# Kernel tuning notes

Hardware: AMD Instinct MI355X
Metric: run time of the kernel (lower is better)

The kernel has to match this reference:

```python
import jax, jax.numpy as jnp
import numpy as np

TOKEN_SELF_ATTN_VALUE = -50000.0
EPS_NORM = 1e-12
EPS_SCATTER = 1e-5
COMMITMENT = 1e-4


def _l2norm(x):
    return x / jnp.maximum(jnp.linalg.norm(x, axis=-1, keepdims=True), EPS_NORM)


def _shift(x):
    # relative-position shift, faithful to the torch `shift` helper
    # x: [..., i, j] -> [..., i, j]
    *pre, i, j = x.shape
    x = jnp.concatenate([x, jnp.zeros((*pre, i, i), x.dtype)], axis=-1)  # [..., i, i+j]
    l = i + j - 1
    x = x.reshape(*pre, i * (i + j))
    pad = (-x.shape[-1]) % l
    x = jnp.concatenate([x, jnp.zeros((*pre, pad), x.dtype)], axis=-1)
    x = x.reshape(*pre, -1, l)
    return x[..., :i, i - 1:]


def setup_inputs() -> dict:
    key = jax.random.key(0)
    k1, k2, k3, k4 = jax.random.split(key, 4)
    b, h, t, d = 4, 8, 8192, 64
    c, wsz = 64, 128
    qk = jax.random.normal(k1, (b, h, t, d), jnp.float32)
    v = jax.random.normal(k2, (b, h, t, d), jnp.float32)
    means = jax.random.normal(k3, (h, c, d), jnp.float32)
    means = _l2norm(means)  # trained kmeans means are unit-normalized
    rel_w = jax.random.normal(k4, (wsz, h, d), jnp.float32) * 0.02
    return {"qk": qk, "v": v, "means": means, "rel_w": rel_w}


def reference(qk, v, means, rel_w):
    b, h, t, d = qk.shape
    c = means.shape[1]
    wsz = min(rel_w.shape[0], t)

    # ---- kmeans routing (eval path: no iterations, fixed means) ----
    k_routing = _l2norm(qk)                                   # [b,h,t,d]
    dists = jnp.einsum('bhld,hcd->bhlc', k_routing, means)    # cosine sims
    buckets = jnp.argmax(dists, axis=-1)                      # [b,h,t]
    # top-wsz tokens per cluster, sorted ascending (matches topk -> sort -> transpose)
    _, idx = jax.lax.top_k(jnp.swapaxes(dists, -1, -2), wsz)  # [b,h,c,wsz]
    indices = jnp.sort(idx, axis=-1).reshape(b, h, c * wsz)   # [b,h,c*wsz]

    # commitment loss against routed means (means is a non-trainable buffer)
    routed_means = means[jnp.arange(h)[None, :, None], buckets]  # [b,h,t,d]
    loss = jnp.mean((k_routing - routed_means) ** 2) * COMMITMENT

    # ---- gather routed windows ----
    qk_g = jnp.take_along_axis(qk, indices[..., None], axis=2).reshape(b, h, c, wsz, d)
    v_g = jnp.take_along_axis(v, indices[..., None], axis=2).reshape(b, h, c, wsz, d)
    q = qk_g
    k = _l2norm(qk_g)

    scale = d ** -0.5
    dots = jnp.einsum('bhnid,bhnjd->bhnij', q, k) * scale     # [b,h,c,wsz,wsz]
    rel = jnp.einsum('bhnid,jhd->bhnij', q, rel_w) * scale
    dots = dots + _shift(rel)

    # token cannot attend to itself within its window
    eye = jnp.eye(wsz, dtype=bool)
    dots = jnp.where(eye, TOKEN_SELF_ATTN_VALUE, dots)

    attn = jax.nn.softmax(dots, axis=-1)
    bo = jnp.einsum('bhnij,bhnjd->bhnid', attn, v_g).reshape(b, h, c * wsz, d)

    # ---- scatter-mean back to original token positions ----
    def scat(idx1, src1):  # idx1: [N], src1: [N,d]
        num = jnp.zeros((t, d), src1.dtype).at[idx1].add(src1)
        den = jnp.zeros((t, d), src1.dtype).at[idx1].add(jnp.ones_like(src1))
        return num / (den + EPS_SCATTER)

    out = jax.vmap(jax.vmap(scat))(indices, bo)               # [b,h,t,d]
    return out, loss
```

## Files before the change

### kernel.cpp

```cpp
#include <hip/hip_runtime.h>
#include <hip/hip_bf16.h>
#include <math.h>

#define NB 4
#define NH 8
#define TT 8192
#define DD 64
#define NC 64
#define WW 128
#define BHN 32
#define SCALE 0.125f
#define INVCAP 24
#define DTPB 64

typedef __bf16  bf16x8 __attribute__((ext_vector_type(8)));
typedef __bf16  bf16x4 __attribute__((ext_vector_type(4)));
typedef float   f32x4  __attribute__((ext_vector_type(4)));
typedef unsigned long long u64;
typedef unsigned int u32;

#define MFMA(a, b, c) __builtin_amdgcn_mfma_f32_16x16x32_bf16((a), (b), (c), 0, 0, 0)

__device__ __forceinline__ u32 monokey(float f) {
    const u32 u = __float_as_uint(f);
    return u ^ (((u32)((int)u >> 31)) | 0x80000000u);
}

__global__ __launch_bounds__(256) void k_prep(
    const float* __restrict__ rel_w, const float* __restrict__ means,
    __bf16* __restrict__ relb, __bf16* __restrict__ msp, float* __restrict__ mn2)
{
    const int b = blockIdx.x, tid = threadIdx.x;
    if (b < 64) {
        const int i = b * 256 + tid;
        const float4 v = ((const float4*)rel_w)[i];
        bf16x4 o;
        o[0] = (__bf16)v.x; o[1] = (__bf16)v.y; o[2] = (__bf16)v.z; o[3] = (__bf16)v.w;
        *(bf16x4*)(relb + i * 4) = o;
    } else {
        const int i = (b - 64) * 256 + tid;
        const float4 v = ((const float4*)means)[i];
        __bf16* mh = msp;
        __bf16* mm = msp + 32768;
        __bf16* ml = msp + 65536;
        float x[4] = {v.x, v.y, v.z, v.w};
        bf16x4 oh, om, ol;
        float ssq = 0.f;
#pragma unroll
        for (int j = 0; j < 4; j++) {
            ssq = fmaf(x[j], x[j], ssq);
            const __bf16 hh_ = (__bf16)x[j];
            const float r1 = x[j] - (float)hh_;
            const __bf16 mm_ = (__bf16)r1;
            const float r2 = r1 - (float)mm_;
            oh[j] = hh_; om[j] = mm_; ol[j] = (__bf16)r2;
        }
        *(bf16x4*)(mh + i * 4) = oh;
        *(bf16x4*)(mm + i * 4) = om;
        *(bf16x4*)(ml + i * 4) = ol;
#pragma unroll
        for (int o = 1; o < 16; o <<= 1) ssq += __shfl_xor(ssq, o);
        if ((tid & 15) == 0) mn2[i >> 4] = ssq;
    }
}

#define QD_ADDR(row, gi) (((row) << 6) + ((((gi) ^ ((row) & 7))) << 3))

__global__ __launch_bounds__(256) void k_dists(
    const float* __restrict__ qk, const __bf16* __restrict__ msp,
    const float* __restrict__ mn2g, u32* __restrict__ keys,
    double* __restrict__ lossa)
{
    __shared__ __attribute__((aligned(16))) __bf16 qh[64 * 64], qm[64 * 64], ql[64 * 64];
    __shared__ __attribute__((aligned(16))) __bf16 ah[64 * 64], am[64 * 64], al[64 * 64];
    __shared__ float invS[DTPB], s2S[DTPB];
    __shared__ double red[4];

    const int bh = blockIdx.x, h = bh & 7, tid = threadIdx.x;
    const int t0 = blockIdx.y * DTPB;

    {
        const bf16x8* sh_ = (const bf16x8*)(msp + h * 4096);
        const bf16x8* sm_ = (const bf16x8*)(msp + 32768 + h * 4096);
        const bf16x8* sl_ = (const bf16x8*)(msp + 65536 + h * 4096);
#pragma unroll
        for (int gg = 0; gg < 2; gg++) {
            const int g = tid + gg * 256;
            const int row = g >> 3, gi = g & 7;
            const int dst = QD_ADDR(row, gi);
            *(bf16x8*)(ah + dst) = sh_[g];
            *(bf16x8*)(am + dst) = sm_[g];
            *(bf16x8*)(al + dst) = sl_[g];
        }
    }
    {
        const int r = tid >> 2, qt = tid & 3;
        const float4* src = (const float4*)(qk + ((size_t)bh * TT + t0 + r) * DD + qt * 16);
        float4 f[4];
        f[0] = src[0]; f[1] = src[1]; f[2] = src[2]; f[3] = src[3];
        bf16x8 vh[2], vm[2], vl[2];
        float ssq = 0.f;
#pragma unroll
        for (int j = 0; j < 16; j++) {
            const float xx = ((const float*)f)[j];
            ssq = fmaf(xx, xx, ssq);
            const __bf16 hh_ = (__bf16)xx;
            const float r1 = xx - (float)hh_;
            const __bf16 mm_ = (__bf16)r1;
            const float r2 = r1 - (float)mm_;
            vh[j >> 3][j & 7] = hh_; vm[j >> 3][j & 7] = mm_; vl[j >> 3][j & 7] = (__bf16)r2;
        }
#pragma unroll
        for (int gg = 0; gg < 2; gg++) {
            const int dst = QD_ADDR(r, qt * 2 + gg);
            *(bf16x8*)(qh + dst) = vh[gg];
            *(bf16x8*)(qm + dst) = vm[gg];
            *(bf16x8*)(ql + dst) = vl[gg];
        }
        ssq += __shfl_xor(ssq, 1);
        ssq += __shfl_xor(ssq, 2);
        if (qt == 0) {
            const float inv = 1.0f / fmaxf(sqrtf(ssq), 1e-12f);
            invS[r] = inv;
            s2S[r] = ssq * inv * inv;
        }
    }
    __syncthreads();

    const int lane = tid & 63, wv = tid >> 6;
    const int lo = lane & 15, quad = lane >> 4;

    bf16x8 Bh[2], Bm[2], Bl[2];
    {
        const int row = wv * 16 + lo;
#pragma unroll
        for (int kh = 0; kh < 2; kh++) {
            const int src = QD_ADDR(row, kh * 4 + quad);
            Bh[kh] = *(const bf16x8*)(qh + src);
            Bm[kh] = *(const bf16x8*)(qm + src);
            Bl[kh] = *(const bf16x8*)(ql + src);
        }
    }

    f32x4 acc[4];
#pragma unroll
    for (int ct = 0; ct < 4; ct++) {
        bf16x8 Ah[2], Am[2], Al[2];
#pragma unroll
        for (int kh = 0; kh < 2; kh++) {
            const int src = QD_ADDR(ct * 16 + lo, kh * 4 + quad);
            Ah[kh] = *(const bf16x8*)(ah + src);
            Am[kh] = *(const bf16x8*)(am + src);
            Al[kh] = *(const bf16x8*)(al + src);
        }
        f32x4 a = (f32x4){0.f, 0.f, 0.f, 0.f};
        a = MFMA(Al[0], Bm[0], a); a = MFMA(Al[1], Bm[1], a);
        a = MFMA(Am[0], Bl[0], a); a = MFMA(Am[1], Bl[1], a);
        a = MFMA(Am[0], Bm[0], a); a = MFMA(Am[1], Bm[1], a);
        a = MFMA(Ah[0], Bl[0], a); a = MFMA(Ah[1], Bl[1], a);
        a = MFMA(Al[0], Bh[0], a); a = MFMA(Al[1], Bh[1], a);
        a = MFMA(Am[0], Bh[0], a); a = MFMA(Am[1], Bh[1], a);
        a = MFMA(Ah[0], Bm[0], a); a = MFMA(Ah[1], Bm[1], a);
        a = MFMA(Ah[0], Bh[0], a); a = MFMA(Ah[1], Bh[1], a);
        acc[ct] = a;
    }

    const int tok = wv * 16 + lo;
    const float inv = invS[tok];
    float rawmax = -3.0e38f; int cbest = 0;
    u32* kout = keys + (size_t)bh * NC * TT + (size_t)(t0 + tok);
#pragma unroll
    for (int ct = 0; ct < 4; ct++)
#pragma unroll
        for (int r = 0; r < 4; r++) {
            const float raw = acc[ct][r];
            const int c = ct * 16 + quad * 4 + r;
            if (raw > rawmax) { rawmax = raw; cbest = c; }
            kout[(size_t)c * TT] = monokey(raw * inv);
        }

#pragma unroll
    for (int off = 16; off < 64; off <<= 1) {
        const float ov = __shfl_xor(rawmax, off);
        const int   oc = __shfl_xor(cbest, off);
        if (ov > rawmax || (ov == rawmax && oc < cbest)) { rawmax = ov; cbest = oc; }
    }
    double lt_lane = 0.0;
    if (quad == 0)
        lt_lane = (double)(s2S[tok] + mn2g[h * 64 + cbest] - 2.0f * rawmax * inv);

#pragma unroll
    for (int o = 32; o; o >>= 1) lt_lane += __shfl_xor(lt_lane, o);
    if (lane == 0) red[wv] = lt_lane;
    __syncthreads();
    if (tid == 0) atomicAdd(lossa, red[0] + red[1] + red[2] + red[3]);
}

__global__ __launch_bounds__(256) void k_topk(
    const u32* __restrict__ keys, int* __restrict__ indices,
    unsigned int* __restrict__ cnt, unsigned short* __restrict__ inv)
{
    __shared__ unsigned int hist[4][256];
    __shared__ int wsum[8];
    __shared__ int bc_bin, bc_rank, bc_cnt;

    const int bhc = blockIdx.x, tid = threadIdx.x;
    const int wv = tid >> 6, lane = tid & 63;
    const int bh = bhc >> 6;

    u32 key[32];
    {
        const uint4* p = (const uint4*)(keys + (size_t)bhc * TT + tid * 32);
#pragma unroll
        for (int i = 0; i < 8; i++) {
            uint4 u = p[i];
            key[4*i] = u.x; key[4*i+1] = u.y; key[4*i+2] = u.z; key[4*i+3] = u.w;
        }
    }

    u32 thr = 0;
    int need = 128, gshift = 24, prevShift = 0;
    unsigned int* hb = &hist[0][0];

    for (int level = 0; level < 4; level++) {
        const int shift = 24 - 8 * level;
        hb[tid] = 0; hb[tid + 256] = 0; hb[tid + 512] = 0; hb[tid + 768] = 0;
        __syncthreads();
        unsigned int* hw = hist[wv];
        if (level == 0) {
#pragma unroll
            for (int i = 0; i < 32; i++)
                atomicAdd(&hw[key[i] >> 24], 1u);
        } else {
            const u32 pv = thr >> prevShift;
#pragma unroll
            for (int i = 0; i < 32; i++)
                if ((key[i] >> prevShift) == pv)
                    atomicAdd(&hw[(key[i] >> shift) & 255u], 1u);
        }
        __syncthreads();

        const int b = 255 - tid;
        const int c = hist[0][b] + hist[1][b] + hist[2][b] + hist[3][b];
        int incl = c;
#pragma unroll
        for (int o = 1; o < 64; o <<= 1) {
            const int v = __shfl_up(incl, o);
            if (lane >= o) incl += v;
        }
        if (lane == 63) wsum[wv] = incl;
        __syncthreads();
        int above = incl - c;
        for (int wj = 0; wj < wv; wj++) above += wsum[wj];
        if (above < need && above + c >= need) {
            bc_bin = b; bc_rank = above; bc_cnt = c;
        }
        __syncthreads();
        thr |= ((u32)bc_bin) << shift;
        need -= bc_rank;
        gshift = shift;
        prevShift = shift;
        if (bc_cnt == need || shift == 0) break;
    }

    const u32 tg = thr >> gshift;
    int cgt = 0, ceq = 0;
#pragma unroll
    for (int i = 0; i < 32; i++) {
        const u32 kg = key[i] >> gshift;
        cgt += (kg > tg) ? 1 : 0;
        ceq += (kg == tg) ? 1 : 0;
    }
    int ig = cgt, ie = ceq;
#pragma unroll
    for (int o = 1; o < 64; o <<= 1) {
        const int vg = __shfl_up(ig, o);
        const int ve = __shfl_up(ie, o);
        if (lane >= o) { ig += vg; ie += ve; }
    }
    if (lane == 63) { wsum[wv] = ig; wsum[4 + wv] = ie; }
    __syncthreads();
    int pgt = ig - cgt, peq = ie - ceq;
    for (int wj = 0; wj < wv; wj++) { pgt += wsum[wj]; peq += wsum[4 + wj]; }

    const int rneed = need;
    int* outp = indices + bhc * WW;
    unsigned int* cntb = cnt + (bh << 13);
    unsigned short* invb = inv + (((size_t)bh << 13) * INVCAP);
    const int cbase = (bhc & 63) * WW;
    int g = 0, e = 0;
#pragma unroll
    for (int i = 0; i < 32; i++) {
        const int tok = tid * 32 + i;
        const u32 kg = key[i] >> gshift;
        if (kg > tg) {
            const int tb = (peq + e < rneed) ? (peq + e) : rneed;
            const int wpos = pgt + g + tb;
            outp[wpos] = tok;
            const unsigned int pos = atomicAdd(&cntb[tok], 1u);
            if (pos < INVCAP) invb[(size_t)tok * INVCAP + pos] = (unsigned short)(cbase + wpos);
            g++;
        } else if (kg == tg) {
            if (peq + e < rneed) {
                const int wpos = pgt + g + peq + e;
                outp[wpos] = tok;
                const unsigned int pos = atomicAdd(&cntb[tok], 1u);
                if (pos < INVCAP) invb[(size_t)tok * INVCAP + pos] = (unsigned short)(cbase + wpos);
            }
            e++;
        }
    }
}

#define QS_ADDR(row, gi) (((row) << 6) + ((((gi) ^ ((row) & 7))) << 3))

__global__ __launch_bounds__(512) void k_attn(
    const float* __restrict__ qk, const float* __restrict__ vin,
    const __bf16* __restrict__ relb, const int* __restrict__ indices,
    float* __restrict__ bo)
{
    __shared__ __attribute__((aligned(16))) __bf16 uv[64 * 136];
    __shared__ __attribute__((aligned(16))) __bf16 rs[128 * 136];
    __shared__ float invs[128];

    const int tid  = threadIdx.x;
    const int lane = tid & 63;
    const int wv   = tid >> 6;
    const int lo   = lane & 15;
    const int quad = lane >> 4;
    const int rbase = wv * 16;

    const int bhc = blockIdx.x;
    const int bh  = bhc >> 6;
    const int h   = bh & 7;

    const int r  = tid >> 2;
    const int qp = tid & 3;
    const int rowidx = indices[bhc * WW + r];
    const size_t rowoff = ((size_t)bh * TT + rowidx) * DD + qp * 16;
    float4 q0, q1, q2, q3, vreg[4];
    {
        const float4* qsrc = (const float4*)(qk + rowoff);
        q0 = qsrc[0]; q1 = qsrc[1]; q2 = qsrc[2]; q3 = qsrc[3];
        const float4* vsrc = (const float4*)(vin + rowoff);
        vreg[0] = vsrc[0]; vreg[1] = vsrc[1]; vreg[2] = vsrc[2]; vreg[3] = vsrc[3];
    }
    {
        float ssq = q0.x*q0.x + q0.y*q0.y + q0.z*q0.z + q0.w*q0.w
                  + q1.x*q1.x + q1.y*q1.y + q1.z*q1.z + q1.w*q1.w
                  + q2.x*q2.x + q2.y*q2.y + q2.z*q2.z + q2.w*q2.w
                  + q3.x*q3.x + q3.y*q3.y + q3.z*q3.z + q3.w*q3.w;
        ssq += __shfl_xor(ssq, 1);
        ssq += __shfl_xor(ssq, 2);
        if (qp == 0) invs[r] = 1.0f / fmaxf(sqrtf(ssq), 1e-12f);
        bf16x8 va, vb;
        va[0]=(__bf16)q0.x; va[1]=(__bf16)q0.y; va[2]=(__bf16)q0.z; va[3]=(__bf16)q0.w;
        va[4]=(__bf16)q1.x; va[5]=(__bf16)q1.y; va[6]=(__bf16)q1.z; va[7]=(__bf16)q1.w;
        vb[0]=(__bf16)q2.x; vb[1]=(__bf16)q2.y; vb[2]=(__bf16)q2.z; vb[3]=(__bf16)q2.w;
        vb[4]=(__bf16)q3.x; vb[5]=(__bf16)q3.y; vb[6]=(__bf16)q3.z; vb[7]=(__bf16)q3.w;
        *(bf16x8*)(uv + QS_ADDR(r, qp * 2))     = va;
        *(bf16x8*)(uv + QS_ADDR(r, qp * 2 + 1)) = vb;
    }
    __syncthreads();

    f32x4 acc[8];

#pragma unroll
    for (int nt = 0; nt < 8; nt++) acc[nt] = (f32x4){0.f, 0.f, 0.f, 0.f};
#pragma unroll
    for (int k0 = 0; k0 < 64; k0 += 32) {
        bf16x8 qa = *(const bf16x8*)(uv + QS_ADDR(rbase + lo, (k0 >> 3) + quad));
#pragma unroll
        for (int nt = 0; nt < 8; nt++) {
            const bf16x8 wb = *(const bf16x8*)(relb + ((nt * 16 + lo) * 8 + h) * 64 + k0 + quad * 8);
            acc[nt] = MFMA(qa, wb, acc[nt]);
        }
    }
#pragma unroll
    for (int nt = 0; nt < 8; nt++)
#pragma unroll
        for (int rg = 0; rg < 4; rg++)
            rs[(rbase + quad * 4 + rg) * 136 + nt * 16 + lo] = (__bf16)acc[nt][rg];

#pragma unroll
    for (int nt = 0; nt < 8; nt++) acc[nt] = (f32x4){0.f, 0.f, 0.f, 0.f};
#pragma unroll
    for (int k0 = 0; k0 < 64; k0 += 32) {
        bf16x8 qa = *(const bf16x8*)(uv + QS_ADDR(rbase + lo, (k0 >> 3) + quad));
#pragma unroll
        for (int nt = 0; nt < 8; nt++) {
            bf16x8 qb = *(const bf16x8*)(uv + QS_ADDR(nt * 16 + lo, (k0 >> 3) + quad));
            acc[nt] = MFMA(qa, qb, acc[nt]);
        }
    }

    float inv_j[8];
#pragma unroll
    for (int nt = 0; nt < 8; nt++) inv_j[nt] = invs[nt * 16 + lo];

#pragma unroll
    for (int rg = 0; rg < 4; rg++) {
        const int i = rbase + quad * 4 + rg;
#pragma unroll
        for (int nt = 0; nt < 8; nt++) {
            const int j = nt * 16 + lo;
            float val = acc[nt][rg] * inv_j[nt] * SCALE;
            if (j <= i) val += SCALE * (float)rs[i * 136 + (j + 127 - i)];
            if (j == i) val = -50000.0f;
            acc[nt][rg] = val;
        }
    }

#pragma unroll
    for (int rg = 0; rg < 4; rg++) {
        float m = -3.0e38f;
#pragma unroll
        for (int nt = 0; nt < 8; nt++) m = fmaxf(m, acc[nt][rg]);
#pragma unroll
        for (int msk = 1; msk < 16; msk <<= 1) m = fmaxf(m, __shfl_xor(m, msk));
        float s = 0.f;
#pragma unroll
        for (int nt = 0; nt < 8; nt++) {
            const float e = __expf(acc[nt][rg] - m);
            acc[nt][rg] = e; s += e;
        }
#pragma unroll
        for (int msk = 1; msk < 16; msk <<= 1) s += __shfl_xor(s, msk);
        const float is = 1.0f / s;
        const int i = rbase + quad * 4 + rg;
#pragma unroll
        for (int nt = 0; nt < 8; nt++)
            rs[i * 136 + nt * 16 + lo] = (__bf16)(acc[nt][rg] * is);
    }
    __syncthreads();

    __bf16* vt = uv;
#pragma unroll
    for (int i = 0; i < 4; i++) {
        vt[(qp * 16 + 4*i + 0) * 136 + r] = (__bf16)vreg[i].x;
        vt[(qp * 16 + 4*i + 1) * 136 + r] = (__bf16)vreg[i].y;
        vt[(qp * 16 + 4*i + 2) * 136 + r] = (__bf16)vreg[i].z;
        vt[(qp * 16 + 4*i + 3) * 136 + r] = (__bf16)vreg[i].w;
    }
    __syncthreads();

    f32x4 accO[4];
#pragma unroll
    for (int nt = 0; nt < 4; nt++) accO[nt] = (f32x4){0.f, 0.f, 0.f, 0.f};
#pragma unroll
    for (int k0 = 0; k0 < 128; k0 += 32) {
        bf16x8 pa = *(const bf16x8*)(rs + (rbase + lo) * 136 + k0 + quad * 8);
#pragma unroll
        for (int nt = 0; nt < 4; nt++) {
            bf16x8 vb = *(const bf16x8*)(vt + (nt * 16 + lo) * 136 + k0 + quad * 8);
            accO[nt] = MFMA(pa, vb, accO[nt]);
        }
    }

    float* bb = bo + (size_t)bhc * (WW * DD);
#pragma unroll
    for (int rg = 0; rg < 4; rg++) {
        const int i = rbase + quad * 4 + rg;
#pragma unroll
        for (int nt = 0; nt < 4; nt++)
            bb[(size_t)i * DD + nt * 16 + lo] = accO[nt][rg];
    }
}

__global__ __launch_bounds__(256) void k_out(
    const float* __restrict__ bo, const unsigned int* __restrict__ cnt,
    const unsigned short* __restrict__ inv, const double* __restrict__ lossa,
    float* __restrict__ out)
{
    const int tid = threadIdx.x;
    const int g = blockIdx.x * 16 + (tid >> 4);
    const int l = tid & 15;
    const int bh = g >> 13;
    const unsigned int n = cnt[g];
    const int nc = (n < (unsigned)INVCAP) ? (int)n : INVCAP;
    const unsigned short* ip = inv + (size_t)g * INVCAP;
    const float* bbase = bo + (((size_t)bh << 13) * DD);
    float4 s = {0.f, 0.f, 0.f, 0.f};
    for (int e = 0; e < nc; e++) {
        const int slot = ip[e];
        float4 v4 = *(const float4*)(bbase + (size_t)slot * DD + l * 4);
        s.x += v4.x; s.y += v4.y; s.z += v4.z; s.w += v4.w;
    }
    const float r = 1.0f / ((float)n + 1e-5f);
    s.x *= r; s.y *= r; s.z *= r; s.w *= r;
    *(float4*)(out + (size_t)g * DD + l * 4) = s;
    if (g == 0 && l == 0) out[16777216] = (float)(lossa[0] * (0.0001 / 16777216.0));
}

extern "C" void kernel_launch(void* const* d_in, const int* in_sizes, int n_in,
                              void* d_out, int out_size, void* d_ws, size_t ws_size,
                              hipStream_t stream) {
    (void)in_sizes; (void)n_in; (void)ws_size; (void)out_size;
    const float* qk    = (const float*)d_in[0];
    const float* v     = (const float*)d_in[1];
    const float* means = (const float*)d_in[2];
    const float* rel_w = (const float*)d_in[3];
    float* out = (float*)d_out;

    char* ws = (char*)d_ws;
    const size_t KEYS_B = (size_t)BHN * NC * TT * 4;
    const size_t IDX_B  = (size_t)BHN * NC * WW * 4;
    const size_t CNT_B  = (size_t)BHN * TT * 4;
    const size_t INV_B  = (size_t)BHN * TT * INVCAP * 2;
    const size_t RELB_B = (size_t)WW * NH * DD * 2;
    u32*            keys  = (u32*)ws;
    float*          bo    = (float*)ws;
    int*            idx   = (int*)(ws + KEYS_B);
    unsigned int*   cnt   = (unsigned int*)(ws + KEYS_B + IDX_B);
    double*         lossa = (double*)(ws + KEYS_B + IDX_B + CNT_B);
    unsigned short* inv   = (unsigned short*)(ws + KEYS_B + IDX_B + CNT_B + 4096);
    __bf16*         relb  = (__bf16*)(ws + KEYS_B + IDX_B + CNT_B + 4096 + INV_B);
    __bf16*         msp   = (__bf16*)(ws + KEYS_B + IDX_B + CNT_B + 4096 + INV_B + RELB_B);
    float*          mn2   = (float*)(ws + KEYS_B + IDX_B + CNT_B + 4096 + INV_B + RELB_B + 196608);

    hipMemsetAsync(ws + KEYS_B + IDX_B, 0, CNT_B + 4096, stream);

    k_prep<<<96, 256, 0, stream>>>(rel_w, means, relb, msp, mn2);
    k_dists<<<dim3(BHN, TT / DTPB), 256, 0, stream>>>(qk, msp, mn2, keys, lossa);
    k_topk<<<BHN * NC, 256, 0, stream>>>(keys, idx, cnt, inv);
    k_attn<<<BHN * NC, 512, 0, stream>>>(qk, v, relb, idx, bo);
    k_out<<<BHN * TT / 16, 256, 0, stream>>>(bo, cnt, inv, lossa, out);
}
```

Measured before the change: 342.9 us.

## Fuse top-k selection into attention kernel and fold workspace zeroing into prep

Merges the radix top-k kernel with the windowed attention kernel, so the selected indices stay in shared memory instead of going through a global index buffer. The histogram is now split into 32 padded sub-histograms, reusing the attention shared-memory buffer, to cut atomic contention with 512 threads. The count and loss zeroing moves from a memset into extra k_prep blocks. The split-bf16 MFMA loop in k_dists is reordered so independent accumulators are interleaved. In exchange, the fused kernel holds more registers and shared memory, which can lower occupancy.

```diff
diff --git a/kernel.cpp b/kernel.cpp
--- a/kernel.cpp
+++ b/kernel.cpp
@@ -28,7 +28,8 @@
 
 __global__ __launch_bounds__(256) void k_prep(
     const float* __restrict__ rel_w, const float* __restrict__ means,
-    __bf16* __restrict__ relb, __bf16* __restrict__ msp, float* __restrict__ mn2)
+    __bf16* __restrict__ relb, __bf16* __restrict__ msp, float* __restrict__ mn2,
+    unsigned int* __restrict__ cnt, double* __restrict__ lossa)
 {
     const int b = blockIdx.x, tid = threadIdx.x;
     if (b < 64) {
@@ -37,7 +38,7 @@
         bf16x4 o;
         o[0] = (__bf16)v.x; o[1] = (__bf16)v.y; o[2] = (__bf16)v.z; o[3] = (__bf16)v.w;
         *(bf16x4*)(relb + i * 4) = o;
-    } else {
+    } else if (b < 96) {
         const int i = (b - 64) * 256 + tid;
         const float4 v = ((const float4*)means)[i];
         __bf16* mh = msp;
@@ -61,6 +62,12 @@
 #pragma unroll
         for (int o = 1; o < 16; o <<= 1) ssq += __shfl_xor(ssq, o);
         if ((tid & 15) == 0) mn2[i >> 4] = ssq;
+    } else {
+        const uint4 z = {0u, 0u, 0u, 0u};
+        uint4* cp = (uint4*)cnt + ((size_t)(b - 96) * 256 + tid) * 8;
+#pragma unroll
+        for (int k = 0; k < 8; k++) cp[k] = z;
+        if (b == 96 && tid == 0) lossa[0] = 0.0;
     }
 }
 
@@ -144,25 +151,32 @@
 
     f32x4 acc[4];
 #pragma unroll
-    for (int ct = 0; ct < 4; ct++) {
-        bf16x8 Ah[2], Am[2], Al[2];
-#pragma unroll
-        for (int kh = 0; kh < 2; kh++) {
-            const int src = QD_ADDR(ct * 16 + lo, kh * 4 + quad);
-            Ah[kh] = *(const bf16x8*)(ah + src);
-            Am[kh] = *(const bf16x8*)(am + src);
-            Al[kh] = *(const bf16x8*)(al + src);
-        }
-        f32x4 a = (f32x4){0.f, 0.f, 0.f, 0.f};
-        a = MFMA(Al[0], Bm[0], a); a = MFMA(Al[1], Bm[1], a);
-        a = MFMA(Am[0], Bl[0], a); a = MFMA(Am[1], Bl[1], a);
-        a = MFMA(Am[0], Bm[0], a); a = MFMA(Am[1], Bm[1], a);
-        a = MFMA(Ah[0], Bl[0], a); a = MFMA(Ah[1], Bl[1], a);
-        a = MFMA(Al[0], Bh[0], a); a = MFMA(Al[1], Bh[1], a);
-        a = MFMA(Am[0], Bh[0], a); a = MFMA(Am[1], Bh[1], a);
-        a = MFMA(Ah[0], Bm[0], a); a = MFMA(Ah[1], Bm[1], a);
-        a = MFMA(Ah[0], Bh[0], a); a = MFMA(Ah[1], Bh[1], a);
-        acc[ct] = a;
+    for (int ct = 0; ct < 4; ct++) acc[ct] = (f32x4){0.f, 0.f, 0.f, 0.f};
+#pragma unroll
+    for (int kh = 0; kh < 2; kh++) {
+        bf16x8 Aa[4], Ab[4];
+#pragma unroll
+        for (int ct = 0; ct < 4; ct++) Aa[ct] = *(const bf16x8*)(ah + QD_ADDR(ct * 16 + lo, kh * 4 + quad));
+#pragma unroll
+        for (int ct = 0; ct < 4; ct++) acc[ct] = MFMA(Aa[ct], Bh[kh], acc[ct]);
+#pragma unroll
+        for (int ct = 0; ct < 4; ct++) Ab[ct] = *(const bf16x8*)(am + QD_ADDR(ct * 16 + lo, kh * 4 + quad));
+#pragma unroll
+        for (int ct = 0; ct < 4; ct++) acc[ct] = MFMA(Aa[ct], Bm[kh], acc[ct]);
+#pragma unroll
+        for (int ct = 0; ct < 4; ct++) acc[ct] = MFMA(Aa[ct], Bl[kh], acc[ct]);
+#pragma unroll
+        for (int ct = 0; ct < 4; ct++) acc[ct] = MFMA(Ab[ct], Bh[kh], acc[ct]);
+#pragma unroll
+        for (int ct = 0; ct < 4; ct++) acc[ct] = MFMA(Ab[ct], Bm[kh], acc[ct]);
+#pragma unroll
+        for (int ct = 0; ct < 4; ct++) acc[ct] = MFMA(Ab[ct], Bl[kh], acc[ct]);
+#pragma unroll
+        for (int ct = 0; ct < 4; ct++) Aa[ct] = *(const bf16x8*)(al + QD_ADDR(ct * 16 + lo, kh * 4 + quad));
+#pragma unroll
+        for (int ct = 0; ct < 4; ct++) acc[ct] = MFMA(Aa[ct], Bh[kh], acc[ct]);
+#pragma unroll
+        for (int ct = 0; ct < 4; ct++) acc[ct] = MFMA(Aa[ct], Bm[kh], acc[ct]);
     }
 
     const int tok = wv * 16 + lo;
@@ -196,64 +210,80 @@
     if (tid == 0) atomicAdd(lossa, red[0] + red[1] + red[2] + red[3]);
 }
 
-__global__ __launch_bounds__(256) void k_topk(
-    const u32* __restrict__ keys, int* __restrict__ indices,
-    unsigned int* __restrict__ cnt, unsigned short* __restrict__ inv)
+#define QS_ADDR(row, gi) (((row) << 6) + ((((gi) ^ ((row) & 7))) << 3))
+
+__global__ __launch_bounds__(512) void k_tka(
+    const u32* __restrict__ keys, const float* __restrict__ qk,
+    const float* __restrict__ vin, const __bf16* __restrict__ relb,
+    unsigned int* __restrict__ cnt, unsigned short* __restrict__ inv,
+    float* __restrict__ bo)
 {
-    __shared__ unsigned int hist[4][256];
-    __shared__ int wsum[8];
-    __shared__ int bc_bin, bc_rank, bc_cnt;
-
-    const int bhc = blockIdx.x, tid = threadIdx.x;
-    const int wv = tid >> 6, lane = tid & 63;
-    const int bh = bhc >> 6;
-
-    u32 key[32];
-    {
-        const uint4* p = (const uint4*)(keys + (size_t)bhc * TT + tid * 32);
-#pragma unroll
-        for (int i = 0; i < 8; i++) {
+    __shared__ __attribute__((aligned(16))) __bf16 uv[64 * 136];
+    __shared__ __attribute__((aligned(16))) __bf16 rs[128 * 136];
+    __shared__ float invs[128];
+    __shared__ int   idxs[128];
+    __shared__ int   wsumA[8], wsumB[8];
+    __shared__ int   bc_bin, bc_rank, bc_cnt;
+
+    unsigned int* hist = (unsigned int*)rs;
+
+    const int tid  = threadIdx.x;
+    const int lane = tid & 63;
+    const int wv   = tid >> 6;
+    const int bhc  = blockIdx.x;
+    const int bh   = bhc >> 6;
+    const int h    = bh & 7;
+
+    u32 key[16];
+    {
+        const uint4* p = (const uint4*)(keys + (size_t)bhc * TT + tid * 16);
+#pragma unroll
+        for (int i = 0; i < 4; i++) {
             uint4 u = p[i];
             key[4*i] = u.x; key[4*i+1] = u.y; key[4*i+2] = u.z; key[4*i+3] = u.w;
         }
     }
-
+    const int cid = tid >> 4;
     u32 thr = 0;
     int need = 128, gshift = 24, prevShift = 0;
-    unsigned int* hb = &hist[0][0];
 
     for (int level = 0; level < 4; level++) {
         const int shift = 24 - 8 * level;
-        hb[tid] = 0; hb[tid + 256] = 0; hb[tid + 512] = 0; hb[tid + 768] = 0;
+        for (int i = tid; i < 32 * 257; i += 512) hist[i] = 0;
         __syncthreads();
-        unsigned int* hw = hist[wv];
+        unsigned int* hc = hist + cid * 257;
         if (level == 0) {
 #pragma unroll
-            for (int i = 0; i < 32; i++)
-                atomicAdd(&hw[key[i] >> 24], 1u);
+            for (int i = 0; i < 16; i++)
+                atomicAdd(&hc[key[i] >> 24], 1u);
         } else {
             const u32 pv = thr >> prevShift;
 #pragma unroll
-            for (int i = 0; i < 32; i++)
+            for (int i = 0; i < 16; i++)
                 if ((key[i] >> prevShift) == pv)
-                    atomicAdd(&hw[(key[i] >> shift) & 255u], 1u);
+                    atomicAdd(&hc[(key[i] >> shift) & 255u], 1u);
         }
         __syncthreads();
-
-        const int b = 255 - tid;
-        const int c = hist[0][b] + hist[1][b] + hist[2][b] + hist[3][b];
-        int incl = c;
-#pragma unroll
-        for (int o = 1; o < 64; o <<= 1) {
-            const int v = __shfl_up(incl, o);
-            if (lane >= o) incl += v;
-        }
-        if (lane == 63) wsum[wv] = incl;
+        int c = 0, incl = 0;
+        if (tid < 256) {
+            const int b = 255 - tid;
+#pragma unroll
+            for (int cc = 0; cc < 32; cc++) c += hist[cc * 257 + b];
+            incl = c;
+#pragma unroll
+            for (int o = 1; o < 64; o <<= 1) {
+                const int v = __shfl_up(incl, o);
+                if (lane >= o) incl += v;
+            }
+            if (lane == 63) wsumA[wv] = incl;
+        }
         __syncthreads();
-        int above = incl - c;
-        for (int wj = 0; wj < wv; wj++) above += wsum[wj];
-        if (above < need && above + c >= need) {
-            bc_bin = b; bc_rank = above; bc_cnt = c;
+        if (tid < 256) {
+            int above = incl - c;
+            for (int wj = 0; wj < wv; wj++) above += wsumA[wj];
+            if (above < need && above + c >= need) {
+                bc_bin = 255 - tid; bc_rank = above; bc_cnt = c;
+            }
         }
         __syncthreads();
         thr |= ((u32)bc_bin) << shift;
@@ -263,80 +293,63 @@
         if (bc_cnt == need || shift == 0) break;
     }
 
-    const u32 tg = thr >> gshift;
-    int cgt = 0, ceq = 0;
-#pragma unroll
-    for (int i = 0; i < 32; i++) {
-        const u32 kg = key[i] >> gshift;
-        cgt += (kg > tg) ? 1 : 0;
-        ceq += (kg == tg) ? 1 : 0;
-    }
-    int ig = cgt, ie = ceq;
-#pragma unroll
-    for (int o = 1; o < 64; o <<= 1) {
-        const int vg = __shfl_up(ig, o);
-        const int ve = __shfl_up(ie, o);
-        if (lane >= o) { ig += vg; ie += ve; }
-    }
-    if (lane == 63) { wsum[wv] = ig; wsum[4 + wv] = ie; }
-    __syncthreads();
-    int pgt = ig - cgt, peq = ie - ceq;
-    for (int wj = 0; wj < wv; wj++) { pgt += wsum[wj]; peq += wsum[4 + wj]; }
-
-    const int rneed = need;
-    int* outp = indices + bhc * WW;
-    unsigned int* cntb = cnt + (bh << 13);
-    unsigned short* invb = inv + (((size_t)bh << 13) * INVCAP);
-    const int cbase = (bhc & 63) * WW;
-    int g = 0, e = 0;
-#pragma unroll
-    for (int i = 0; i < 32; i++) {
-        const int tok = tid * 32 + i;
-        const u32 kg = key[i] >> gshift;
-        if (kg > tg) {
-            const int tb = (peq + e < rneed) ? (peq + e) : rneed;
-            const int wpos = pgt + g + tb;
-            outp[wpos] = tok;
-            const unsigned int pos = atomicAdd(&cntb[tok], 1u);
-            if (pos < INVCAP) invb[(size_t)tok * INVCAP + pos] = (unsigned short)(cbase + wpos);
-            g++;
-        } else if (kg == tg) {
-            if (peq + e < rneed) {
-                const int wpos = pgt + g + peq + e;
-                outp[wpos] = tok;
+    {
+        const u32 tg = thr >> gshift;
+        int cgt = 0, ceq = 0;
+#pragma unroll
+        for (int i = 0; i < 16; i++) {
+            const u32 kg = key[i] >> gshift;
+            cgt += (kg > tg) ? 1 : 0;
+            ceq += (kg == tg) ? 1 : 0;
+        }
+        int ig = cgt, ie = ceq;
+#pragma unroll
+        for (int o = 1; o < 64; o <<= 1) {
+            const int vg = __shfl_up(ig, o);
+            const int ve = __shfl_up(ie, o);
+            if (lane >= o) { ig += vg; ie += ve; }
+        }
+        if (lane == 63) { wsumA[wv] = ig; wsumB[wv] = ie; }
+        __syncthreads();
+        int pgt = ig - cgt, peq = ie - ceq;
+        for (int wj = 0; wj < wv; wj++) { pgt += wsumA[wj]; peq += wsumB[wj]; }
+
+        const int rneed = need;
+        unsigned int* cntb = cnt + (bh << 13);
+        unsigned short* invb = inv + (((size_t)bh << 13) * INVCAP);
+        const int cbase = (bhc & 63) * WW;
+        int g = 0, e = 0;
+#pragma unroll
+        for (int i = 0; i < 16; i++) {
+            const int tok = tid * 16 + i;
+            const u32 kg = key[i] >> gshift;
+            if (kg > tg) {
+                const int tb = (peq + e < rneed) ? (peq + e) : rneed;
+                const int wpos = pgt + g + tb;
+                idxs[wpos] = tok;
                 const unsigned int pos = atomicAdd(&cntb[tok], 1u);
                 if (pos < INVCAP) invb[(size_t)tok * INVCAP + pos] = (unsigned short)(cbase + wpos);
+                g++;
+            } else if (kg == tg) {
+                if (peq + e < rneed) {
+                    const int wpos = pgt + g + peq + e;
+                    idxs[wpos] = tok;
+                    const unsigned int pos = atomicAdd(&cntb[tok], 1u);
+                    if (pos < INVCAP) invb[(size_t)tok * INVCAP + pos] = (unsigned short)(cbase + wpos);
+                }
+                e++;
             }
-            e++;
-        }
-    }
-}
-
-#define QS_ADDR(row, gi) (((row) << 6) + ((((gi) ^ ((row) & 7))) << 3))
-
-__global__ __launch_bounds__(512) void k_attn(
-    const float* __restrict__ qk, const float* __restrict__ vin,
-    const __bf16* __restrict__ relb, const int* __restrict__ indices,
-    float* __restrict__ bo)
-{
-    __shared__ __attribute__((aligned(16))) __bf16 uv[64 * 136];
-    __shared__ __attribute__((aligned(16))) __bf16 rs[128 * 136];
-    __shared__ float invs[128];
-
-    const int tid  = threadIdx.x;
-    const int lane = tid & 63;
-    const int wv   = tid >> 6;
+        }
+    }
+    __syncthreads();
+
     const int lo   = lane & 15;
     const int quad = lane >> 4;
     const int rbase = wv * 16;
 
-    const int bhc = blockIdx.x;
-    const int bh  = bhc >> 6;
-    const int h   = bh & 7;
-
     const int r  = tid >> 2;
     const int qp = tid & 3;
-    const int rowidx = indices[bhc * WW + r];
+    const int rowidx = idxs[r];
     const size_t rowoff = ((size_t)bh * TT + rowidx) * DD + qp * 16;
     float4 q0, q1, q2, q3, vreg[4];
     {
@@ -504,25 +517,20 @@
 
     char* ws = (char*)d_ws;
     const size_t KEYS_B = (size_t)BHN * NC * TT * 4;
-    const size_t IDX_B  = (size_t)BHN * NC * WW * 4;
     const size_t CNT_B  = (size_t)BHN * TT * 4;
     const size_t INV_B  = (size_t)BHN * TT * INVCAP * 2;
     const size_t RELB_B = (size_t)WW * NH * DD * 2;
     u32*            keys  = (u32*)ws;
     float*          bo    = (float*)ws;
-    int*            idx   = (int*)(ws + KEYS_B);
-    unsigned int*   cnt   = (unsigned int*)(ws + KEYS_B + IDX_B);
-    double*         lossa = (double*)(ws + KEYS_B + IDX_B + CNT_B);
-    unsigned short* inv   = (unsigned short*)(ws + KEYS_B + IDX_B + CNT_B + 4096);
-    __bf16*         relb  = (__bf16*)(ws + KEYS_B + IDX_B + CNT_B + 4096 + INV_B);
-    __bf16*         msp   = (__bf16*)(ws + KEYS_B + IDX_B + CNT_B + 4096 + INV_B + RELB_B);
-    float*          mn2   = (float*)(ws + KEYS_B + IDX_B + CNT_B + 4096 + INV_B + RELB_B + 196608);
-
-    hipMemsetAsync(ws + KEYS_B + IDX_B, 0, CNT_B + 4096, stream);
-
-    k_prep<<<96, 256, 0, stream>>>(rel_w, means, relb, msp, mn2);
+    unsigned int*   cnt   = (unsigned int*)(ws + KEYS_B);
+    double*         lossa = (double*)(ws + KEYS_B + CNT_B);
+    unsigned short* inv   = (unsigned short*)(ws + KEYS_B + CNT_B + 4096);
+    __bf16*         relb  = (__bf16*)(ws + KEYS_B + CNT_B + 4096 + INV_B);
+    __bf16*         msp   = (__bf16*)(ws + KEYS_B + CNT_B + 4096 + INV_B + RELB_B);
+    float*          mn2   = (float*)(ws + KEYS_B + CNT_B + 4096 + INV_B + RELB_B + 196608);
+
+    k_prep<<<128, 256, 0, stream>>>(rel_w, means, relb, msp, mn2, cnt, lossa);
     k_dists<<<dim3(BHN, TT / DTPB), 256, 0, stream>>>(qk, msp, mn2, keys, lossa);
-    k_topk<<<BHN * NC, 256, 0, stream>>>(keys, idx, cnt, inv);
-    k_attn<<<BHN * NC, 512, 0, stream>>>(qk, v, relb, idx, bo);
+    k_tka<<<BHN * NC, 512, 0, stream>>>(keys, qk, v, relb, cnt, inv, bo);
     k_out<<<BHN * TT / 16, 256, 0, stream>>>(bo, cnt, inv, lossa, out);
 }
```

New measurement: 348.9 us. About the same (+1.7%).

## Fold prep kernel into dists and batch scatter-mean gathers in k_out

Applied to the files above, without the earlier changes.

Removes the separate k_prep launch. Each k_dists block now splits the means into three bf16 parts and computes their squared norms itself, keeping them in shared memory, while blocks with blockIdx.y==0 convert rel_w to bf16 for the attention kernel. k_out loads the first eight inverse slot indices with one vector load and issues up to eight independent gathers before summing, which exposes more memory-level parallelism. The cost is redundant means conversion in every dists block and a different floating-point summation order.

```diff
diff --git a/kernel.cpp b/kernel.cpp
--- a/kernel.cpp
+++ b/kernel.cpp
@@ -26,72 +26,60 @@
     return u ^ (((u32)((int)u >> 31)) | 0x80000000u);
 }
 
-__global__ __launch_bounds__(256) void k_prep(
-    const float* __restrict__ rel_w, const float* __restrict__ means,
-    __bf16* __restrict__ relb, __bf16* __restrict__ msp, float* __restrict__ mn2)
-{
-    const int b = blockIdx.x, tid = threadIdx.x;
-    if (b < 64) {
-        const int i = b * 256 + tid;
-        const float4 v = ((const float4*)rel_w)[i];
-        bf16x4 o;
-        o[0] = (__bf16)v.x; o[1] = (__bf16)v.y; o[2] = (__bf16)v.z; o[3] = (__bf16)v.w;
-        *(bf16x4*)(relb + i * 4) = o;
-    } else {
-        const int i = (b - 64) * 256 + tid;
-        const float4 v = ((const float4*)means)[i];
-        __bf16* mh = msp;
-        __bf16* mm = msp + 32768;
-        __bf16* ml = msp + 65536;
-        float x[4] = {v.x, v.y, v.z, v.w};
-        bf16x4 oh, om, ol;
-        float ssq = 0.f;
-#pragma unroll
-        for (int j = 0; j < 4; j++) {
-            ssq = fmaf(x[j], x[j], ssq);
-            const __bf16 hh_ = (__bf16)x[j];
-            const float r1 = x[j] - (float)hh_;
-            const __bf16 mm_ = (__bf16)r1;
-            const float r2 = r1 - (float)mm_;
-            oh[j] = hh_; om[j] = mm_; ol[j] = (__bf16)r2;
-        }
-        *(bf16x4*)(mh + i * 4) = oh;
-        *(bf16x4*)(mm + i * 4) = om;
-        *(bf16x4*)(ml + i * 4) = ol;
-#pragma unroll
-        for (int o = 1; o < 16; o <<= 1) ssq += __shfl_xor(ssq, o);
-        if ((tid & 15) == 0) mn2[i >> 4] = ssq;
-    }
-}
-
 #define QD_ADDR(row, gi) (((row) << 6) + ((((gi) ^ ((row) & 7))) << 3))
 
 __global__ __launch_bounds__(256) void k_dists(
-    const float* __restrict__ qk, const __bf16* __restrict__ msp,
-    const float* __restrict__ mn2g, u32* __restrict__ keys,
-    double* __restrict__ lossa)
+    const float* __restrict__ qk, const float* __restrict__ means,
+    const float* __restrict__ rel_w, __bf16* __restrict__ relb,
+    u32* __restrict__ keys, double* __restrict__ lossa)
 {
     __shared__ __attribute__((aligned(16))) __bf16 qh[64 * 64], qm[64 * 64], ql[64 * 64];
     __shared__ __attribute__((aligned(16))) __bf16 ah[64 * 64], am[64 * 64], al[64 * 64];
-    __shared__ float invS[DTPB], s2S[DTPB];
+    __shared__ float invS[DTPB], s2S[DTPB], mn2S[NC];
     __shared__ double red[4];
 
     const int bh = blockIdx.x, h = bh & 7, tid = threadIdx.x;
     const int t0 = blockIdx.y * DTPB;
 
+    if (blockIdx.y == 0) {
+        const float4* rw = (const float4*)rel_w;
+#pragma unroll
+        for (int k = 0; k < 2; k++) {
+            const int i = bh * 512 + k * 256 + tid;
+            const float4 v = rw[i];
+            bf16x4 o;
+            o[0] = (__bf16)v.x; o[1] = (__bf16)v.y; o[2] = (__bf16)v.z; o[3] = (__bf16)v.w;
+            *(bf16x4*)(relb + i * 4) = o;
+        }
+    }
+
     {
-        const bf16x8* sh_ = (const bf16x8*)(msp + h * 4096);
-        const bf16x8* sm_ = (const bf16x8*)(msp + 32768 + h * 4096);
-        const bf16x8* sl_ = (const bf16x8*)(msp + 65536 + h * 4096);
+        const int r = tid >> 2, qt = tid & 3;
+        const float4* src = (const float4*)(means + (size_t)(h * NC + r) * DD + qt * 16);
+        float4 f[4];
+        f[0] = src[0]; f[1] = src[1]; f[2] = src[2]; f[3] = src[3];
+        bf16x8 vh[2], vm[2], vl[2];
+        float ssq = 0.f;
+#pragma unroll
+        for (int j = 0; j < 16; j++) {
+            const float xx = ((const float*)f)[j];
+            ssq = fmaf(xx, xx, ssq);
+            const __bf16 hh_ = (__bf16)xx;
+            const float r1 = xx - (float)hh_;
+            const __bf16 mm_ = (__bf16)r1;
+            const float r2 = r1 - (float)mm_;
+            vh[j >> 3][j & 7] = hh_; vm[j >> 3][j & 7] = mm_; vl[j >> 3][j & 7] = (__bf16)r2;
+        }
 #pragma unroll
         for (int gg = 0; gg < 2; gg++) {
-            const int g = tid + gg * 256;
-            const int row = g >> 3, gi = g & 7;
-            const int dst = QD_ADDR(row, gi);
-            *(bf16x8*)(ah + dst) = sh_[g];
-            *(bf16x8*)(am + dst) = sm_[g];
-            *(bf16x8*)(al + dst) = sl_[g];
-        }
+            const int dst = QD_ADDR(r, qt * 2 + gg);
+            *(bf16x8*)(ah + dst) = vh[gg];
+            *(bf16x8*)(am + dst) = vm[gg];
+            *(bf16x8*)(al + dst) = vl[gg];
+        }
+        ssq += __shfl_xor(ssq, 1);
+        ssq += __shfl_xor(ssq, 2);
+        if (qt == 0) mn2S[r] = ssq;
     }
     {
         const int r = tid >> 2, qt = tid & 3;
@@ -187,7 +175,7 @@
     }
     double lt_lane = 0.0;
     if (quad == 0)
-        lt_lane = (double)(s2S[tok] + mn2g[h * 64 + cbest] - 2.0f * rawmax * inv);
+        lt_lane = (double)(s2S[tok] + mn2S[cbest] - 2.0f * rawmax * inv);
 
 #pragma unroll
     for (int o = 32; o; o >>= 1) lt_lane += __shfl_xor(lt_lane, o);
@@ -479,13 +467,37 @@
     const unsigned int n = cnt[g];
     const int nc = (n < (unsigned)INVCAP) ? (int)n : INVCAP;
     const unsigned short* ip = inv + (size_t)g * INVCAP;
-    const float* bbase = bo + (((size_t)bh << 13) * DD);
-    float4 s = {0.f, 0.f, 0.f, 0.f};
-    for (int e = 0; e < nc; e++) {
+    const float* bbase = bo + (((size_t)bh << 13) * DD) + l * 4;
+
+    const uint4 ipv = *(const uint4*)ip;
+    const int s0 = ipv.x & 0xffff, s1 = ipv.x >> 16;
+    const int s2 = ipv.y & 0xffff, s3 = ipv.y >> 16;
+    const int s4 = ipv.z & 0xffff, s5 = ipv.z >> 16;
+    const int s6 = ipv.w & 0xffff, s7 = ipv.w >> 16;
+
+    float4 a0 = {0.f,0.f,0.f,0.f}, a1 = a0, a2 = a0, a3 = a0;
+    float4 a4 = a0, a5 = a0, a6 = a0, a7 = a0;
+    if (nc > 0) a0 = *(const float4*)(bbase + (size_t)s0 * DD);
+    if (nc > 1) a1 = *(const float4*)(bbase + (size_t)s1 * DD);
+    if (nc > 2) a2 = *(const float4*)(bbase + (size_t)s2 * DD);
+    if (nc > 3) a3 = *(const float4*)(bbase + (size_t)s3 * DD);
+    if (nc > 4) a4 = *(const float4*)(bbase + (size_t)s4 * DD);
+    if (nc > 5) a5 = *(const float4*)(bbase + (size_t)s5 * DD);
+    if (nc > 6) a6 = *(const float4*)(bbase + (size_t)s6 * DD);
+    if (nc > 7) a7 = *(const float4*)(bbase + (size_t)s7 * DD);
+
+    float4 s;
+    s.x = ((a0.x + a1.x) + (a2.x + a3.x)) + ((a4.x + a5.x) + (a6.x + a7.x));
+    s.y = ((a0.y + a1.y) + (a2.y + a3.y)) + ((a4.y + a5.y) + (a6.y + a7.y));
+    s.z = ((a0.z + a1.z) + (a2.z + a3.z)) + ((a4.z + a5.z) + (a6.z + a7.z));
+    s.w = ((a0.w + a1.w) + (a2.w + a3.w)) + ((a4.w + a5.w) + (a6.w + a7.w));
+
+    for (int e = 8; e < nc; e++) {
         const int slot = ip[e];
-        float4 v4 = *(const float4*)(bbase + (size_t)slot * DD + l * 4);
+        const float4 v4 = *(const float4*)(bbase + (size_t)slot * DD);
         s.x += v4.x; s.y += v4.y; s.z += v4.z; s.w += v4.w;
     }
+
     const float r = 1.0f / ((float)n + 1e-5f);
     s.x *= r; s.y *= r; s.z *= r; s.w *= r;
     *(float4*)(out + (size_t)g * DD + l * 4) = s;
@@ -507,7 +519,6 @@
     const size_t IDX_B  = (size_t)BHN * NC * WW * 4;
     const size_t CNT_B  = (size_t)BHN * TT * 4;
     const size_t INV_B  = (size_t)BHN * TT * INVCAP * 2;
-    const size_t RELB_B = (size_t)WW * NH * DD * 2;
     u32*            keys  = (u32*)ws;
     float*          bo    = (float*)ws;
     int*            idx   = (int*)(ws + KEYS_B);
@@ -515,13 +526,10 @@
     double*         lossa = (double*)(ws + KEYS_B + IDX_B + CNT_B);
     unsigned short* inv   = (unsigned short*)(ws + KEYS_B + IDX_B + CNT_B + 4096);
     __bf16*         relb  = (__bf16*)(ws + KEYS_B + IDX_B + CNT_B + 4096 + INV_B);
-    __bf16*         msp   = (__bf16*)(ws + KEYS_B + IDX_B + CNT_B + 4096 + INV_B + RELB_B);
-    float*          mn2   = (float*)(ws + KEYS_B + IDX_B + CNT_B + 4096 + INV_B + RELB_B + 196608);
 
     hipMemsetAsync(ws + KEYS_B + IDX_B, 0, CNT_B + 4096, stream);
 
-    k_prep<<<96, 256, 0, stream>>>(rel_w, means, relb, msp, mn2);
-    k_dists<<<dim3(BHN, TT / DTPB), 256, 0, stream>>>(qk, msp, mn2, keys, lossa);
+    k_dists<<<dim3(BHN, TT / DTPB), 256, 0, stream>>>(qk, means, rel_w, relb, keys, lossa);
     k_topk<<<BHN * NC, 256, 0, stream>>>(keys, idx, cnt, inv);
     k_attn<<<BHN * NC, 512, 0, stream>>>(qk, v, relb, idx, bo);
     k_out<<<BHN * TT / 16, 256, 0, stream>>>(bo, cnt, inv, lossa, out);
```

Result: no change. 336.7 us (-1.8%).
